# Performance work log

Measured on AMD Instinct MI355X. Metric: run time of the kernel, lower is better.

## Reference

```python
import jax, jax.numpy as jnp
import numpy as np
from itertools import product

B, D, H, W_, C = 2, 64, 64, 64, 96
OUT = 192  # c_multiplier * dim
EPS = 1e-5


def setup_inputs() -> dict:
    key = jax.random.key(0)
    k1, k2 = jax.random.split(key)
    x = jax.random.normal(k1, (B, D, H, W_, C), dtype=jnp.float32)
    ln_w = jnp.ones((8 * C,), dtype=jnp.float32)
    ln_b = jnp.zeros((8 * C,), dtype=jnp.float32)
    W = jax.random.normal(k2, (OUT, 8 * C), dtype=jnp.float32) * 0.02
    return {"x": x, "ln_w": ln_w, "ln_b": ln_b, "W": W}


def reference(x, ln_w, ln_b, W):
    # strided patch gather + concat: order matches itertools.product over (0,1)^3
    parts = [x[:, s0::2, s1::2, s2::2, :] for s0, s1, s2 in product((0, 1), repeat=3)]
    y = jnp.concatenate(parts, axis=-1)  # [B, D/2, H/2, W/2, 8C]
    # LayerNorm over last dim
    mu = jnp.mean(y, axis=-1, keepdims=True)
    var = jnp.mean(jnp.square(y - mu), axis=-1, keepdims=True)
    y = (y - mu) * jax.lax.rsqrt(var + EPS) * ln_w + ln_b
    # linear reduction (bias=False); torch Linear weight is [out, in]
    return jnp.einsum('bdhwc,oc->bdhwo', y, W)
```

## Files before the change

### kernel.cpp

```cpp
#include <hip/hip_runtime.h>
#include <stdint.h>

#define C_IN   96
#define KIN    768
#define NOUT   192
#define MTILE  32
#define LDK    772
#define EPS    1e-5f

typedef __bf16 bf16x8 __attribute__((ext_vector_type(8)));
typedef float  f32x4  __attribute__((ext_vector_type(4)));

static __device__ __forceinline__ unsigned int f2bf(float f) {
    union { float f; unsigned int u; } v; v.f = f;
    return (v.u + 0x7fffu + ((v.u >> 16) & 1u)) >> 16;
}
static __device__ __forceinline__ float bf2f(unsigned int s) {
    union { unsigned int u; float f; } v; v.u = s << 16;
    return v.f;
}

__global__ __launch_bounds__(256) void prep_kernel(
    const float* __restrict__ W, const float* __restrict__ lnw,
    const float* __restrict__ lnb, unsigned short* __restrict__ Wb,
    float* __restrict__ bias, float* __restrict__ Scol)
{
    int o = blockIdx.x;
    int tid = threadIdx.x;
    float bpart = 0.f, spart = 0.f;
    for (int c = tid; c < KIN; c += 256) {
        float w = W[(size_t)o * KIN + c];
        unsigned int rb = f2bf(w * lnw[c]);
        Wb[(size_t)o * KIN + c] = (unsigned short)rb;
        spart += bf2f(rb);
        bpart += w * lnb[c];
    }
    #pragma unroll
    for (int m = 32; m >= 1; m >>= 1) {
        bpart += __shfl_xor(bpart, m, 64);
        spart += __shfl_xor(spart, m, 64);
    }
    __shared__ float redb[4], reds[4];
    if ((tid & 63) == 0) { redb[tid >> 6] = bpart; reds[tid >> 6] = spart; }
    __syncthreads();
    if (tid == 0) {
        bias[o] = redb[0] + redb[1] + redb[2] + redb[3];
        Scol[o] = reds[0] + reds[1] + reds[2] + reds[3];
    }
}

__global__ __launch_bounds__(256, 3) void merge_kernel(
    const float* __restrict__ x, const unsigned short* __restrict__ Wb,
    const float* __restrict__ bias, const float* __restrict__ Scol,
    float* __restrict__ out)
{
    __shared__ unsigned short ylds[MTILE * LDK];
    __shared__ float muL[MTILE], rsL[MTILE];

    const int tid   = threadIdx.x;
    const int tbase = blockIdx.x * MTILE;
    const int bh = blockIdx.x;
    const int h  = bh & 31;
    const int d  = (bh >> 5) & 31;
    const int b  = bh >> 10;

    const int tk = tid >> 3;
    const int i  = tid & 7;
    const float* base = x +
        ((size_t)((b * 64 + 2 * d) * 64 + 2 * h) * 64 + 2 * tk) * C_IN + i * 4;

    const int OFF[8] = {0, 96, 6144, 6240, 393216, 393312, 399360, 399456};

    float4 v[24];
    #pragma unroll
    for (int g = 0; g < 8; ++g)
        #pragma unroll
        for (int jj = 0; jj < 3; ++jj)
            v[g * 3 + jj] = *(const float4*)(base + OFF[g] + jj * 32);

    float sum = 0.f, sq = 0.f;
    #pragma unroll
    for (int g = 0; g < 8; ++g) {
        #pragma unroll
        for (int jj = 0; jj < 3; ++jj) {
            float4 t = v[g * 3 + jj];
            sum += t.x + t.y + t.z + t.w;
            sq  += t.x * t.x + t.y * t.y + t.z * t.z + t.w * t.w;
            uint2 p;
            p.x = f2bf(t.x) | (f2bf(t.y) << 16);
            p.y = f2bf(t.z) | (f2bf(t.w) << 16);
            *(uint2*)&ylds[tk * LDK + g * 96 + (i + jj * 8) * 4] = p;
        }
    }
    #pragma unroll
    for (int m = 4; m >= 1; m >>= 1) {
        sum += __shfl_xor(sum, m, 8);
        sq  += __shfl_xor(sq,  m, 8);
    }
    if (i == 0) {
        float mean = sum * (1.f / 768.f);
        float var  = sq * (1.f / 768.f) - mean * mean;
        muL[tk] = mean;
        rsL[tk] = rsqrtf(var + EPS);
    }
    __syncthreads();

    const int wv    = tid >> 6;
    const int l     = tid & 63;
    const int l15   = l & 15;
    const int quad  = l >> 4;
    const int nbase = wv * 48;
    const int koff  = quad * 8;

    f32x4 acc[2][3];
    #pragma unroll
    for (int mt = 0; mt < 2; ++mt)
        #pragma unroll
        for (int nt = 0; nt < 3; ++nt)
            acc[mt][nt] = (f32x4){0.f, 0.f, 0.f, 0.f};

    const unsigned short* arow0 = &ylds[l15        * LDK + koff];
    const unsigned short* arow1 = &ylds[(16 + l15) * LDK + koff];
    const unsigned short* brow0 = Wb + (size_t)(nbase + l15) * KIN + koff;
    const unsigned short* brow1 = brow0 + 16 * KIN;
    const unsigned short* brow2 = brow0 + 32 * KIN;

    bf16x8 a0 = *(const bf16x8*)arow0;
    bf16x8 a1 = *(const bf16x8*)arow1;
    bf16x8 b0 = *(const bf16x8*)brow0;
    bf16x8 b1 = *(const bf16x8*)brow1;
    bf16x8 b2 = *(const bf16x8*)brow2;
    #pragma unroll
    for (int kk = 0; kk < 24; ++kk) {
        bf16x8 na0, na1, nb0, nb1, nb2;
        if (kk < 23) {
            const int k = (kk + 1) * 32;
            na0 = *(const bf16x8*)(arow0 + k);
            na1 = *(const bf16x8*)(arow1 + k);
            nb0 = *(const bf16x8*)(brow0 + k);
            nb1 = *(const bf16x8*)(brow1 + k);
            nb2 = *(const bf16x8*)(brow2 + k);
        }
        acc[0][0] = __builtin_amdgcn_mfma_f32_16x16x32_bf16(a0, b0, acc[0][0], 0, 0, 0);
        acc[0][1] = __builtin_amdgcn_mfma_f32_16x16x32_bf16(a0, b1, acc[0][1], 0, 0, 0);
        acc[0][2] = __builtin_amdgcn_mfma_f32_16x16x32_bf16(a0, b2, acc[0][2], 0, 0, 0);
        acc[1][0] = __builtin_amdgcn_mfma_f32_16x16x32_bf16(a1, b0, acc[1][0], 0, 0, 0);
        acc[1][1] = __builtin_amdgcn_mfma_f32_16x16x32_bf16(a1, b1, acc[1][1], 0, 0, 0);
        acc[1][2] = __builtin_amdgcn_mfma_f32_16x16x32_bf16(a1, b2, acc[1][2], 0, 0, 0);
        a0 = na0; a1 = na1; b0 = nb0; b1 = nb1; b2 = nb2;
    }

    const float S0 = Scol[nbase + l15];
    const float S1 = Scol[nbase + 16 + l15];
    const float S2 = Scol[nbase + 32 + l15];
    const float c0 = bias[nbase + l15];
    const float c1 = bias[nbase + 16 + l15];
    const float c2 = bias[nbase + 32 + l15];
    #pragma unroll
    for (int mt = 0; mt < 2; ++mt) {
        #pragma unroll
        for (int r = 0; r < 4; ++r) {
            const int row = mt * 16 + quad * 4 + r;
            const float rs = rsL[row];
            const float rm = rs * muL[row];
            float* op = out + (size_t)(tbase + row) * NOUT + nbase + l15;
            op[0]  = rs * acc[mt][0][r] - rm * S0 + c0;
            op[16] = rs * acc[mt][1][r] - rm * S1 + c1;
            op[32] = rs * acc[mt][2][r] - rm * S2 + c2;
        }
    }
}

extern "C" void kernel_launch(void* const* d_in, const int* in_sizes, int n_in,
                              void* d_out, int out_size, void* d_ws, size_t ws_size,
                              hipStream_t stream) {
    const float* x   = (const float*)d_in[0];
    const float* lnw = (const float*)d_in[1];
    const float* lnb = (const float*)d_in[2];
    const float* W   = (const float*)d_in[3];
    float* out = (float*)d_out;

    unsigned short* Wb = (unsigned short*)d_ws;
    float* bias = (float*)((char*)d_ws + (size_t)NOUT * KIN * 2);
    float* Scol = bias + NOUT;

    prep_kernel<<<NOUT, 256, 0, stream>>>(W, lnw, lnb, Wb, bias, Scol);
    merge_kernel<<<2048, 256, 0, stream>>>(x, Wb, bias, Scol, out);
}
```

Before: 345.7 us.

## Pre-swizzle weights into MFMA fragment order and double-buffer operand prefetch

The bf16 weight conversion moves into a separate kernel that writes W in per-lane MFMA fragment order, so each wave's B-operand loads become fully contiguous 1KB chunks per k-step instead of strided row reads. The K loop now prefetches two steps ahead with double-buffered register operands, and a sched_barrier keeps all global x loads issued before the LayerNorm math. This adds an extra small prep launch and more live registers, which could pressure occupancy at the 3-blocks launch bound.

```diff
diff --git a/kernel.cpp b/kernel.cpp
--- a/kernel.cpp
+++ b/kernel.cpp
@@ -7,6 +7,7 @@
 #define MTILE  32
 #define LDK    772
 #define EPS    1e-5f
+#define NKIT   24
 
 typedef __bf16 bf16x8 __attribute__((ext_vector_type(8)));
 typedef float  f32x4  __attribute__((ext_vector_type(4)));
@@ -20,19 +21,17 @@
     return v.f;
 }
 
-__global__ __launch_bounds__(256) void prep_kernel(
+__global__ __launch_bounds__(256) void prep_bias(
     const float* __restrict__ W, const float* __restrict__ lnw,
-    const float* __restrict__ lnb, unsigned short* __restrict__ Wb,
-    float* __restrict__ bias, float* __restrict__ Scol)
+    const float* __restrict__ lnb, float* __restrict__ bias,
+    float* __restrict__ Scol)
 {
     int o = blockIdx.x;
     int tid = threadIdx.x;
     float bpart = 0.f, spart = 0.f;
     for (int c = tid; c < KIN; c += 256) {
         float w = W[(size_t)o * KIN + c];
-        unsigned int rb = f2bf(w * lnw[c]);
-        Wb[(size_t)o * KIN + c] = (unsigned short)rb;
-        spart += bf2f(rb);
+        spart += bf2f(f2bf(w * lnw[c]));
         bpart += w * lnb[c];
     }
     #pragma unroll
@@ -49,8 +48,31 @@
     }
 }
 
+__global__ __launch_bounds__(256) void prep_swz(
+    const float* __restrict__ W, const float* __restrict__ lnw,
+    unsigned short* __restrict__ Wsw)
+{
+    const int nt = blockIdx.x;
+    for (int s = threadIdx.x; s < NKIT * 64; s += 256) {
+        const int kk = s >> 6;
+        const int l  = s & 63;
+        const int row = nt * 16 + (l & 15);
+        const int k0  = kk * 32 + (l >> 4) * 8;
+        const float* src = W + (size_t)row * KIN + k0;
+        unsigned int p[4];
+        #pragma unroll
+        for (int j = 0; j < 4; ++j) {
+            float a = src[2 * j]     * lnw[k0 + 2 * j];
+            float b = src[2 * j + 1] * lnw[k0 + 2 * j + 1];
+            p[j] = f2bf(a) | (f2bf(b) << 16);
+        }
+        *(uint4*)&Wsw[(size_t)((nt * NKIT + kk) * 64 + l) * 8] =
+            make_uint4(p[0], p[1], p[2], p[3]);
+    }
+}
+
 __global__ __launch_bounds__(256, 3) void merge_kernel(
-    const float* __restrict__ x, const unsigned short* __restrict__ Wb,
+    const float* __restrict__ x, const unsigned short* __restrict__ Wsw,
     const float* __restrict__ bias, const float* __restrict__ Scol,
     float* __restrict__ out)
 {
@@ -77,6 +99,8 @@
         #pragma unroll
         for (int jj = 0; jj < 3; ++jj)
             v[g * 3 + jj] = *(const float4*)(base + OFF[g] + jj * 32);
+
+    __builtin_amdgcn_sched_barrier(0);
 
     float sum = 0.f, sq = 0.f;
     #pragma unroll
@@ -121,33 +145,40 @@
 
     const unsigned short* arow0 = &ylds[l15        * LDK + koff];
     const unsigned short* arow1 = &ylds[(16 + l15) * LDK + koff];
-    const unsigned short* brow0 = Wb + (size_t)(nbase + l15) * KIN + koff;
-    const unsigned short* brow1 = brow0 + 16 * KIN;
-    const unsigned short* brow2 = brow0 + 32 * KIN;
-
-    bf16x8 a0 = *(const bf16x8*)arow0;
-    bf16x8 a1 = *(const bf16x8*)arow1;
-    bf16x8 b0 = *(const bf16x8*)brow0;
-    bf16x8 b1 = *(const bf16x8*)brow1;
-    bf16x8 b2 = *(const bf16x8*)brow2;
-    #pragma unroll
-    for (int kk = 0; kk < 24; ++kk) {
+    const unsigned short* bp0 = Wsw + ((size_t)((3 * wv + 0) * NKIT) * 64 + l) * 8;
+    const unsigned short* bp1 = Wsw + ((size_t)((3 * wv + 1) * NKIT) * 64 + l) * 8;
+    const unsigned short* bp2 = Wsw + ((size_t)((3 * wv + 2) * NKIT) * 64 + l) * 8;
+
+    bf16x8 A0[2], A1[2], B0[2], B1[2], B2[2];
+    #pragma unroll
+    for (int p = 0; p < 2; ++p) {
+        A0[p] = *(const bf16x8*)(arow0 + p * 32);
+        A1[p] = *(const bf16x8*)(arow1 + p * 32);
+        B0[p] = *(const bf16x8*)(bp0 + p * 512);
+        B1[p] = *(const bf16x8*)(bp1 + p * 512);
+        B2[p] = *(const bf16x8*)(bp2 + p * 512);
+    }
+    #pragma unroll
+    for (int kk = 0; kk < NKIT; ++kk) {
+        const int c = kk & 1;
         bf16x8 na0, na1, nb0, nb1, nb2;
-        if (kk < 23) {
-            const int k = (kk + 1) * 32;
-            na0 = *(const bf16x8*)(arow0 + k);
-            na1 = *(const bf16x8*)(arow1 + k);
-            nb0 = *(const bf16x8*)(brow0 + k);
-            nb1 = *(const bf16x8*)(brow1 + k);
-            nb2 = *(const bf16x8*)(brow2 + k);
-        }
-        acc[0][0] = __builtin_amdgcn_mfma_f32_16x16x32_bf16(a0, b0, acc[0][0], 0, 0, 0);
-        acc[0][1] = __builtin_amdgcn_mfma_f32_16x16x32_bf16(a0, b1, acc[0][1], 0, 0, 0);
-        acc[0][2] = __builtin_amdgcn_mfma_f32_16x16x32_bf16(a0, b2, acc[0][2], 0, 0, 0);
-        acc[1][0] = __builtin_amdgcn_mfma_f32_16x16x32_bf16(a1, b0, acc[1][0], 0, 0, 0);
-        acc[1][1] = __builtin_amdgcn_mfma_f32_16x16x32_bf16(a1, b1, acc[1][1], 0, 0, 0);
-        acc[1][2] = __builtin_amdgcn_mfma_f32_16x16x32_bf16(a1, b2, acc[1][2], 0, 0, 0);
-        a0 = na0; a1 = na1; b0 = nb0; b1 = nb1; b2 = nb2;
+        if (kk < NKIT - 2) {
+            const int k2 = kk + 2;
+            na0 = *(const bf16x8*)(arow0 + k2 * 32);
+            na1 = *(const bf16x8*)(arow1 + k2 * 32);
+            nb0 = *(const bf16x8*)(bp0 + k2 * 512);
+            nb1 = *(const bf16x8*)(bp1 + k2 * 512);
+            nb2 = *(const bf16x8*)(bp2 + k2 * 512);
+        }
+        acc[0][0] = __builtin_amdgcn_mfma_f32_16x16x32_bf16(A0[c], B0[c], acc[0][0], 0, 0, 0);
+        acc[0][1] = __builtin_amdgcn_mfma_f32_16x16x32_bf16(A0[c], B1[c], acc[0][1], 0, 0, 0);
+        acc[0][2] = __builtin_amdgcn_mfma_f32_16x16x32_bf16(A0[c], B2[c], acc[0][2], 0, 0, 0);
+        acc[1][0] = __builtin_amdgcn_mfma_f32_16x16x32_bf16(A1[c], B0[c], acc[1][0], 0, 0, 0);
+        acc[1][1] = __builtin_amdgcn_mfma_f32_16x16x32_bf16(A1[c], B1[c], acc[1][1], 0, 0, 0);
+        acc[1][2] = __builtin_amdgcn_mfma_f32_16x16x32_bf16(A1[c], B2[c], acc[1][2], 0, 0, 0);
+        if (kk < NKIT - 2) {
+            A0[c] = na0; A1[c] = na1; B0[c] = nb0; B1[c] = nb1; B2[c] = nb2;
+        }
     }
 
     const float S0 = Scol[nbase + l15];
@@ -180,10 +211,11 @@
     const float* W   = (const float*)d_in[3];
     float* out = (float*)d_out;
 
-    unsigned short* Wb = (unsigned short*)d_ws;
+    unsigned short* Wsw = (unsigned short*)d_ws;
     float* bias = (float*)((char*)d_ws + (size_t)NOUT * KIN * 2);
     float* Scol = bias + NOUT;
 
-    prep_kernel<<<NOUT, 256, 0, stream>>>(W, lnw, lnb, Wb, bias, Scol);
-    merge_kernel<<<2048, 256, 0, stream>>>(x, Wb, bias, Scol, out);
-}
+    prep_bias<<<NOUT, 256, 0, stream>>>(W, lnw, lnb, bias, Scol);
+    prep_swz<<<12, 256, 0, stream>>>(W, lnw, Wsw);
+    merge_kernel<<<2048, 256, 0, stream>>>(x, Wsw, bias, Scol, out);
+}
```

Result: faster. 324.1 us (-6.2%).
